# Optimization experiments

Measured on AMD Instinct MI355X. Metric: run time of the kernel, lower is better.

Reference implementation:

```python
import jax, jax.numpy as jnp
import numpy as np

B, N, IN_DIM, HID, EMB, E = 64, 2048, 128, 256, 64, 4194304
TOTAL = B * N


def _init(key, shape, fan_in):
    return jax.random.normal(key, shape, jnp.float32) / np.sqrt(fan_in).astype(np.float32)


def setup_inputs() -> dict:
    key = jax.random.key(0)
    ks = jax.random.split(key, 9)
    x = jax.random.normal(ks[0], (TOTAL, IN_DIM), jnp.float32)
    src = jax.random.randint(ks[1], (E,), 0, TOTAL)
    dst = jax.random.randint(ks[2], (E,), 0, TOTAL)
    return {
        "x": x,
        "src": src,
        "dst": dst,
        "num_nodes": TOTAL,
        "nodes_per_graph": N,
        "w_lin": _init(ks[3], (IN_DIM, HID), IN_DIM),
        "b_lin": jnp.zeros((HID,), jnp.float32),
        "w_c0": _init(ks[4], (HID, HID), HID),
        "b_c0": jnp.zeros((HID,), jnp.float32),
        "w_c1": _init(ks[5], (HID, HID), HID),
        "b_c1": jnp.zeros((HID,), jnp.float32),
        "w_emb": _init(ks[6], (HID, EMB), HID),
        "b_emb": jnp.zeros((EMB,), jnp.float32),
    }


def reference(x, src, dst, num_nodes, nodes_per_graph,
              w_lin, b_lin, w_c0, b_c0, w_c1, b_c1, w_emb, b_emb):
    # DGL GraphConv norm='both': deg clamped to min 1, symmetric normalization
    ones = jnp.ones(src.shape, x.dtype)
    out_deg = jax.ops.segment_sum(ones, src, num_segments=num_nodes)
    in_deg = jax.ops.segment_sum(ones, dst, num_segments=num_nodes)
    out_norm = jnp.maximum(out_deg, 1.0) ** -0.5  # [num_nodes]
    in_norm = jnp.maximum(in_deg, 1.0) ** -0.5

    def graph_conv(h, W, b):
        hs = h * out_norm[:, None]                                   # pre-norm by out-degree
        agg = jax.ops.segment_sum(hs[src], dst, num_segments=num_nodes)  # SpMM: sum messages
        return (agg * in_norm[:, None]) @ W + b                      # post-norm, then weight

    h = jax.nn.relu(x @ w_lin + b_lin)          # [total, HID]
    h = jax.nn.relu(graph_conv(h, w_c0, b_c0))  # residual=False for agg_style='node'
    h = jax.nn.relu(graph_conv(h, w_c1, b_c1))
    # agent node 0 of each graph in the batch: indices 0, N, 2N, ...
    agent = h[jnp.arange(0, num_nodes, nodes_per_graph)]  # [B, HID]
    return agent @ w_emb + b_emb                          # [B, EMB]
```

## Files before the change

kernel.cpp:

```cpp
#include <hip/hip_runtime.h>
#include <hip/hip_bf16.h>

#define TOTAL_N   131072
#define NEDGE     4194304
#define NPG       2048
#define IN_DIM_K  128
#define HID_K     256
#define EMB_K     64
#define NAGENT    64

#define F1CAP     4096
#define APACK     128
#define BCAP      96

#define G1        256
#define EPB1      (NEDGE / G1)
#define HWORDS    (TOTAL_N / 8)

#define SELB      256
#define EPB       (NEDGE / SELB)


#define ZERO_SPAN 34048

typedef float f32x4 __attribute__((ext_vector_type(4)));
typedef short bf16x8 __attribute__((ext_vector_type(8)));

__device__ inline unsigned short f2bf(float f) {
    unsigned int u = __float_as_uint(f);
    return (unsigned short)((u + 0x7FFFu + ((u >> 16) & 1u)) >> 16);
}

__global__ __launch_bounds__(1024) void k_outdeg_e0(
    const int* __restrict__ src, const int* __restrict__ dst,
    unsigned int* __restrict__ partial,
    unsigned int* __restrict__ bitmap,
    int* __restrict__ e0pack, int* __restrict__ e0cnt)
{
    __shared__ unsigned int hist[HWORDS];
    int t = threadIdx.x;
    #pragma unroll
    for (int i = 0; i < HWORDS / 1024; i++) hist[t + i * 1024] = 0u;
    __syncthreads();

    int ebase = blockIdx.x * EPB1;
    const int4* s4 = (const int4*)(src + ebase);
    const int4* d4 = (const int4*)(dst + ebase);
    #pragma unroll
    for (int i = 0; i < EPB1 / 4096; i++) {
        int4 sv = s4[i * 1024 + t];
        int4 dv = d4[i * 1024 + t];
        int ss[4] = {sv.x, sv.y, sv.z, sv.w};
        int dd[4] = {dv.x, dv.y, dv.z, dv.w};
        #pragma unroll
        for (int j = 0; j < 4; j++) {
            int s = ss[j], d = dd[j];
            atomicAdd(&hist[s >> 3], 1u << ((s & 7) * 4));
            if ((d & (NPG - 1)) == 0) {
                atomicOr(&bitmap[s >> 5], 1u << (s & 31));
                int a = d >> 11;
                int slot = atomicAdd(&e0cnt[a], 1);
                if (slot < APACK) e0pack[a * APACK + slot] = s;
            }
        }
    }
    __syncthreads();
    unsigned int* pout = partial + blockIdx.x * HWORDS;
    #pragma unroll
    for (int i = 0; i < HWORDS / 1024; i++) pout[t + i * 1024] = hist[t + i * 1024];
}

__global__ __launch_bounds__(1024) void k_auxred(
    const unsigned int* __restrict__ bitmap, int* __restrict__ loc,
    int* __restrict__ counters,
    const unsigned int* __restrict__ partial, unsigned int* __restrict__ out_deg,
    const float* __restrict__ wlin, unsigned short* __restrict__ wswz)
{
    int b = blockIdx.x;
    int t = threadIdx.x;
    if (b < 128) {
        __shared__ int cnt, gbase;
        if (t == 0) cnt = 0;
        __syncthreads();
        int v = b * 1024 + t;
        int f = (bitmap[v >> 5] >> (v & 31)) & 1u;
        int p = -1;
        if (f) p = atomicAdd(&cnt, 1);
        __syncthreads();
        if (t == 0) gbase = cnt ? atomicAdd(&counters[1], cnt) : 0;
        __syncthreads();
        int l = -1;
        if (p >= 0) { int id = gbase + p; if (id < F1CAP) l = id; }
        loc[v] = l;
    } else if (b < 256) {
        __shared__ unsigned int redE[8][128], redO[8][128];
        int wl = t & 127, gs = t >> 7;
        int w = (b - 128) * 128 + wl;
        unsigned int accE = 0, accO = 0;
        #pragma unroll 8
        for (int i = 0; i < 32; i++) {
            unsigned int v = partial[(gs * 32 + i) * HWORDS + w];
            accE += v & 0x0F0F0F0Fu;
            accO += (v >> 4) & 0x0F0F0F0Fu;
        }
        redE[gs][wl] = accE;
        redO[gs][wl] = accO;
        __syncthreads();
        if (gs == 0) {
            unsigned int sE = 0, sO = 0;
            #pragma unroll
            for (int j = 0; j < 8; j++) { sE += redE[j][wl]; sO += redO[j][wl]; }
            uint4 lo = make_uint4(sE & 255u, sO & 255u, (sE >> 8) & 255u, (sO >> 8) & 255u);
            uint4 hi = make_uint4((sE >> 16) & 255u, (sO >> 16) & 255u, (sE >> 24) & 255u, (sO >> 24) & 255u);
            ((uint4*)(out_deg + 8 * w))[0] = lo;
            ((uint4*)(out_deg + 8 * w))[1] = hi;
        }
    } else {
        int g = (b - 256) * 1024 + t;
        int lane = g & 63, ct = (g >> 6) & 15, kt = g >> 10;
        int colbase = ct * 16 + (lane & 15);
        int kbase = kt * 32 + (lane >> 4) * 8;
        unsigned short o[8];
        #pragma unroll
        for (int i = 0; i < 8; i++) o[i] = f2bf(wlin[(kbase + i) * HID_K + colbase]);
        *(ushort4*)(wswz + g * 8)     = make_ushort4(o[0], o[1], o[2], o[3]);
        *(ushort4*)(wswz + g * 8 + 4) = make_ushort4(o[4], o[5], o[6], o[7]);
    }
}

__global__ __launch_bounds__(1024) void k_e1_select(
    const int* __restrict__ src, const int* __restrict__ dst,
    const int* __restrict__ loc, const unsigned int* __restrict__ bitmap,
    int* __restrict__ inF1, int* __restrict__ es_bucket)
{
    __shared__ unsigned int bm[TOTAL_N / 32];
    int t = threadIdx.x;
    ((uint4*)bm)[t] = ((const uint4*)bitmap)[t];
    __syncthreads();

    int ebase = blockIdx.x * EPB;
    const int4* d4p = (const int4*)(dst + ebase);
    #pragma unroll
    for (int i = 0; i < EPB / 4096; i++) {
        int4 d4 = d4p[i * 1024 + t];
        int eidx = ebase + (i * 1024 + t) * 4;
        int dd[4] = {d4.x, d4.y, d4.z, d4.w};
        #pragma unroll
        for (int j = 0; j < 4; j++) {
            int d = dd[j];
            if ((bm[d >> 5] >> (d & 31)) & 1u) {
                int l = loc[d];
                if (l >= 0) {
                    int slot = atomicAdd(&inF1[l], 1);
                    if (slot < BCAP) es_bucket[l * BCAP + slot] = src[eidx + j];
                }
            }
        }
    }
}

__global__ __launch_bounds__(256) void k_h0agg(
    const float* __restrict__ x, const unsigned short* __restrict__ wswz,
    const float* __restrict__ blin, const int* __restrict__ es_bucket,
    const unsigned int* __restrict__ out_deg, const int* __restrict__ inF1,
    const int* __restrict__ counters, float* __restrict__ agg1)
{
    __shared__ unsigned short A[3 * 32][136];
    __shared__ float escs[3 * 32];
    __shared__ int rsrc[3 * 32];

    int nF1 = min(counters[1], F1CAP);
    int l = blockIdx.x;
    if (l >= nF1) return;
    int cnt = min(inF1[l], BCAP);
    int ntile = (cnt + 31) >> 5;
    int t = threadIdx.x;
    int lane = t & 63, wq = t >> 6;
    int cbase = lane & 15, rgrp = (lane >> 4) * 4;

    if (t < 96) {
        int s = (t < cnt) ? es_bucket[l * BCAP + t] : -1;
        rsrc[t] = s;
        escs[t] = (s >= 0) ? rsqrtf((float)max((int)out_deg[s], 1)) : 0.f;
    }
    __syncthreads();

    int nslots = (ntile * 32) * 32;
    for (int idx = t; idx < nslots; idx += 256) {
        int r = idx >> 5, q = idx & 31;
        int s = rsrc[r];
        float4 v = make_float4(0.f, 0.f, 0.f, 0.f);
        if (s >= 0) v = ((const float4*)(x + (long long)s * IN_DIM_K))[q];
        ushort4 h;
        h.x = f2bf(v.x); h.y = f2bf(v.y); h.z = f2bf(v.z); h.w = f2bf(v.w);
        *(ushort4*)&A[r][q * 4] = h;
    }
    __syncthreads();

    float bj[4];
    #pragma unroll
    for (int n = 0; n < 4; n++) bj[n] = blin[wq * 64 + n * 16 + cbase];

    float colacc[4] = {0.f, 0.f, 0.f, 0.f};

    for (int ti = 0; ti < ntile; ti++) {
        f32x4 acc[2][4];
        #pragma unroll
        for (int m = 0; m < 2; m++)
            #pragma unroll
            for (int n = 0; n < 4; n++) acc[m][n] = (f32x4){0.f, 0.f, 0.f, 0.f};

        const unsigned short* Ab = &A[ti * 32][0];
        #pragma unroll
        for (int kt = 0; kt < 4; kt++) {
            bf16x8 a0 = *(const bf16x8*)(Ab + ((lane & 15) * 136 + kt * 32 + (lane >> 4) * 8));
            bf16x8 a1 = *(const bf16x8*)(Ab + (((lane & 15) + 16) * 136 + kt * 32 + (lane >> 4) * 8));
            #pragma unroll
            for (int n = 0; n < 4; n++) {
                bf16x8 bf = *(const bf16x8*)(wswz + ((kt * 16 + wq * 4 + n) * 64 + lane) * 8);
                acc[0][n] = __builtin_amdgcn_mfma_f32_16x16x32_bf16(a0, bf, acc[0][n], 0, 0, 0);
                acc[1][n] = __builtin_amdgcn_mfma_f32_16x16x32_bf16(a1, bf, acc[1][n], 0, 0, 0);
            }
        }

        #pragma unroll
        for (int n = 0; n < 4; n++) {
            float part = 0.f;
            #pragma unroll
            for (int m = 0; m < 2; m++)
                #pragma unroll
                for (int j = 0; j < 4; j++) {
                    int row = m * 16 + rgrp + j;
                    part += fmaxf(acc[m][n][j] + bj[n], 0.f) * escs[ti * 32 + row];
                }
            part += __shfl_xor(part, 16);
            part += __shfl_xor(part, 32);
            colacc[n] += part;
        }
    }

    if (lane < 16) {
        #pragma unroll
        for (int n = 0; n < 4; n++)
            agg1[(long long)l * HID_K + wq * 64 + n * 16 + lane] = colacc[n];
    }
}

__global__ __launch_bounds__(256) void k_h1(
    const float* __restrict__ agg1, const float* __restrict__ wc0,
    const float* __restrict__ bc0,
    const int* __restrict__ inF1,
    const int* __restrict__ counters, float* __restrict__ h1)
{
    __shared__ float as[16][HID_K];
    __shared__ float ns[16];

    int nF1 = min(counters[1], F1CAP);
    int base = blockIdx.x * 16;
    if (base >= nF1) return;
    int t = threadIdx.x;

    if (t < 16) {
        int l = base + t;
        ns[t] = (l < nF1) ? rsqrtf((float)max(inF1[l], 1)) : 0.f;
    }
    __syncthreads();

    #pragma unroll
    for (int i = 0; i < 4; i++) {
        int idx = t + i * 256;
        int e = idx >> 6;
        int q = idx & 63;
        int l = base + e;
        float4 v = make_float4(0.f, 0.f, 0.f, 0.f);
        if (l < nF1) v = ((const float4*)(agg1 + (long long)l * HID_K))[q];
        float sc = ns[e];
        v.x *= sc; v.y *= sc; v.z *= sc; v.w *= sc;
        ((float4*)as[e])[q] = v;
    }
    __syncthreads();

    float acc[16];
    #pragma unroll
    for (int e = 0; e < 16; e++) acc[e] = 0.f;

    int j = t;
    for (int k = 0; k < HID_K; k += 4) {
        float w0 = wc0[(k + 0) * HID_K + j];
        float w1 = wc0[(k + 1) * HID_K + j];
        float w2 = wc0[(k + 2) * HID_K + j];
        float w3 = wc0[(k + 3) * HID_K + j];
        #pragma unroll
        for (int e = 0; e < 16; e++) {
            float4 av = *(const float4*)&as[e][k];
            acc[e] = fmaf(av.x, w0, acc[e]);
            acc[e] = fmaf(av.y, w1, acc[e]);
            acc[e] = fmaf(av.z, w2, acc[e]);
            acc[e] = fmaf(av.w, w3, acc[e]);
        }
    }

    float bj = bc0[j];
    #pragma unroll
    for (int e = 0; e < 16; e++) {
        int l = base + e;
        if (l < nF1) h1[(long long)l * HID_K + j] = fmaxf(acc[e] + bj, 0.f);
    }
}

__global__ __launch_bounds__(256) void k_final(
    const int* __restrict__ e0pack, const int* __restrict__ e0cnt,
    const int* __restrict__ loc, const unsigned int* __restrict__ out_deg,
    const float* __restrict__ h1,
    const float* __restrict__ wc1, const float* __restrict__ bc1,
    const float* __restrict__ wemb, const float* __restrict__ bemb,
    float* __restrict__ out)
{
    __shared__ float a_s[HID_K];
    __shared__ float h2[HID_K];
    __shared__ int   ls[APACK];
    __shared__ float scs[APACK];
    int a = blockIdx.x;
    int t = threadIdx.x;

    int n0 = e0cnt[a];
    int ne = min(n0, APACK);
    if (t < ne) {
        int s = e0pack[a * APACK + t];
        int l = loc[s];
        ls[t] = l;
        scs[t] = (l >= 0) ? rsqrtf((float)max((int)out_deg[s], 1)) : 0.f;
    }
    __syncthreads();

    float acc = 0.f;
    for (int i = 0; i < ne; i++) {
        int l = ls[i];
        if (l >= 0) acc = fmaf(scs[i], h1[(long long)l * HID_K + t], acc);
    }
    a_s[t] = acc * rsqrtf((float)max(n0, 1));
    __syncthreads();

    float h = 0.f;
    for (int k = 0; k < HID_K; k++)
        h = fmaf(a_s[k], wc1[k * HID_K + t], h);
    h2[t] = fmaxf(h + bc1[t], 0.f);
    __syncthreads();

    if (t < EMB_K) {
        float o = bemb[t];
        for (int k = 0; k < HID_K; k++)
            o = fmaf(h2[k], wemb[k * EMB_K + t], o);
        out[a * EMB_K + t] = o;
    }
}

extern "C" void kernel_launch(void* const* d_in, const int* in_sizes, int n_in,
                              void* d_out, int out_size, void* d_ws, size_t ws_size,
                              hipStream_t stream)
{
    const float* x    = (const float*)d_in[0];
    const int*   src  = (const int*)d_in[1];
    const int*   dst  = (const int*)d_in[2];
    const float* wlin = (const float*)d_in[5];
    const float* blin = (const float*)d_in[6];
    const float* wc0  = (const float*)d_in[7];
    const float* bc0  = (const float*)d_in[8];
    const float* wc1  = (const float*)d_in[9];
    const float* bc1  = (const float*)d_in[10];
    const float* wemb = (const float*)d_in[11];
    const float* bemb = (const float*)d_in[12];
    float* out = (float*)d_out;

    char* ws = (char*)d_ws;
    int*            counters  = (int*)(ws + 0);
    int*            inF1      = (int*)(ws + 1024);
    int*            e0cnt     = (int*)(ws + 17408);
    unsigned int*   bitmap    = (unsigned int*)(ws + 17664);
    int*            loc       = (int*)(ws + 65536);
    int*            e0pack    = (int*)(ws + 589824);
    int*            es_bucket = (int*)(ws + 622592);
    unsigned int*   out_deg   = (unsigned int*)(ws + 2195456);
    unsigned short* wswz      = (unsigned short*)(ws + 2719744);
    float*          h1        = (float*)(ws + 2785280);
    float*          agg1      = (float*)(ws + 6979584);
    unsigned int*   partial   = (unsigned int*)(ws + 11173888);

    hipMemsetAsync(ws, 0, ZERO_SPAN, stream);

    k_outdeg_e0<<<G1, 1024, 0, stream>>>(src, dst, partial, bitmap, e0pack, e0cnt);
    k_auxred<<<260, 1024, 0, stream>>>(bitmap, loc, counters,
                                       partial, out_deg, wlin, wswz);
    k_e1_select<<<SELB, 1024, 0, stream>>>(src, dst, loc, bitmap,
                                           inF1, es_bucket);
    k_h0agg<<<F1CAP, 256, 0, stream>>>(x, wswz, blin, es_bucket, out_deg,
                                       inF1, counters, agg1);
    k_h1<<<F1CAP / 16, 256, 0, stream>>>(agg1, wc0, bc0, inF1, counters, h1);
    k_final<<<NAGENT, 256, 0, stream>>>(e0pack, e0cnt, loc, out_deg, h1,
                                        wc1, bc1, wemb, bemb, out);
}
```

Baseline: 117.0 us.

## Deduplicate layer-0 source nodes before computing h0, then gather-aggregate

Instead of computing the first linear layer once per incoming edge of each frontier node, the selection pass now marks unique source nodes in a second bitmap. A new compaction kernel assigns them dense ids. h0 is then computed once per unique source into a global buffer, and a separate kernel sums the pre-normalised rows per frontier node. This removes repeated MFMA work and x reads for sources shared by several edges. In exchange it adds atomicOr traffic, two extra launches, and a large intermediate h0 buffer that must be written and then gathered back.

```diff
diff --git a/kernel.cpp b/kernel.cpp
--- a/kernel.cpp
+++ b/kernel.cpp
@@ -10,6 +10,7 @@
 #define NAGENT    64
 
 #define F1CAP     4096
+#define F2CAP     81920
 #define APACK     128
 #define BCAP      96
 
@@ -21,7 +22,7 @@
 #define EPB       (NEDGE / SELB)
 
 
-#define ZERO_SPAN 34048
+#define ZERO_SPAN 50304
 
 typedef float f32x4 __attribute__((ext_vector_type(4)));
 typedef short bf16x8 __attribute__((ext_vector_type(8)));
@@ -131,7 +132,8 @@
 __global__ __launch_bounds__(1024) void k_e1_select(
     const int* __restrict__ src, const int* __restrict__ dst,
     const int* __restrict__ loc, const unsigned int* __restrict__ bitmap,
-    int* __restrict__ inF1, int* __restrict__ es_bucket)
+    int* __restrict__ inF1, int* __restrict__ es_bucket,
+    unsigned int* __restrict__ bitmap2)
 {
     __shared__ unsigned int bm[TOTAL_N / 32];
     int t = threadIdx.x;
@@ -151,99 +153,138 @@
             if ((bm[d >> 5] >> (d & 31)) & 1u) {
                 int l = loc[d];
                 if (l >= 0) {
+                    int s = src[eidx + j];
+                    atomicOr(&bitmap2[s >> 5], 1u << (s & 31));
                     int slot = atomicAdd(&inF1[l], 1);
-                    if (slot < BCAP) es_bucket[l * BCAP + slot] = src[eidx + j];
+                    if (slot < BCAP) es_bucket[l * BCAP + slot] = s;
                 }
             }
         }
     }
 }
 
-__global__ __launch_bounds__(256) void k_h0agg(
+__global__ __launch_bounds__(1024) void k_compact2(
+    const unsigned int* __restrict__ bitmap2, int* __restrict__ loc2,
+    int* __restrict__ nodeOf2, int* __restrict__ counters)
+{
+    __shared__ int cnt, gbase;
+    int t = threadIdx.x;
+    if (t == 0) cnt = 0;
+    __syncthreads();
+    int v = blockIdx.x * 1024 + t;
+    int f = (bitmap2[v >> 5] >> (v & 31)) & 1u;
+    int p = -1;
+    if (f) p = atomicAdd(&cnt, 1);
+    __syncthreads();
+    if (t == 0) gbase = cnt ? atomicAdd(&counters[2], cnt) : 0;
+    __syncthreads();
+    int l = -1;
+    if (p >= 0) {
+        int id = gbase + p;
+        if (id < F2CAP) { l = id; nodeOf2[id] = v; }
+    }
+    loc2[v] = l;
+}
+
+__global__ __launch_bounds__(256) void k_h0f2(
     const float* __restrict__ x, const unsigned short* __restrict__ wswz,
-    const float* __restrict__ blin, const int* __restrict__ es_bucket,
-    const unsigned int* __restrict__ out_deg, const int* __restrict__ inF1,
+    const float* __restrict__ blin, const int* __restrict__ nodeOf2,
+    const unsigned int* __restrict__ out_deg, const int* __restrict__ counters,
+    float* __restrict__ h0f2)
+{
+    __shared__ unsigned short A[32][136];
+    __shared__ float escs[32];
+    __shared__ int rsrc[32];
+
+    int nF2 = min(counters[2], F2CAP);
+    int base = blockIdx.x * 32;
+    if (base >= nF2) return;
+    int t = threadIdx.x;
+    int lane = t & 63, wq = t >> 6;
+    int cbase = lane & 15, rgrp = (lane >> 4) * 4;
+
+    if (t < 32) {
+        int r = base + t;
+        int s = (r < nF2) ? nodeOf2[r] : -1;
+        rsrc[t] = s;
+        escs[t] = (s >= 0) ? rsqrtf((float)max((int)out_deg[s], 1)) : 0.f;
+    }
+    __syncthreads();
+
+    #pragma unroll
+    for (int i = 0; i < 4; i++) {
+        int idx = t + i * 256;
+        int rr = idx >> 5, q = idx & 31;
+        int s = rsrc[rr];
+        float4 v = make_float4(0.f, 0.f, 0.f, 0.f);
+        if (s >= 0) v = ((const float4*)(x + (long long)s * IN_DIM_K))[q];
+        ushort4 h;
+        h.x = f2bf(v.x); h.y = f2bf(v.y); h.z = f2bf(v.z); h.w = f2bf(v.w);
+        *(ushort4*)&A[rr][q * 4] = h;
+    }
+    __syncthreads();
+
+    f32x4 acc[2][4];
+    #pragma unroll
+    for (int m = 0; m < 2; m++)
+        #pragma unroll
+        for (int n = 0; n < 4; n++) acc[m][n] = (f32x4){0.f, 0.f, 0.f, 0.f};
+
+    const unsigned short* Ab = &A[0][0];
+    #pragma unroll
+    for (int kt = 0; kt < 4; kt++) {
+        bf16x8 a0 = *(const bf16x8*)(Ab + ((lane & 15) * 136 + kt * 32 + (lane >> 4) * 8));
+        bf16x8 a1 = *(const bf16x8*)(Ab + (((lane & 15) + 16) * 136 + kt * 32 + (lane >> 4) * 8));
+        #pragma unroll
+        for (int n = 0; n < 4; n++) {
+            bf16x8 bf = *(const bf16x8*)(wswz + ((kt * 16 + wq * 4 + n) * 64 + lane) * 8);
+            acc[0][n] = __builtin_amdgcn_mfma_f32_16x16x32_bf16(a0, bf, acc[0][n], 0, 0, 0);
+            acc[1][n] = __builtin_amdgcn_mfma_f32_16x16x32_bf16(a1, bf, acc[1][n], 0, 0, 0);
+        }
+    }
+
+    #pragma unroll
+    for (int n = 0; n < 4; n++) {
+        float bj = blin[wq * 64 + n * 16 + cbase];
+        #pragma unroll
+        for (int m = 0; m < 2; m++)
+            #pragma unroll
+            for (int j = 0; j < 4; j++) {
+                int row = m * 16 + rgrp + j;
+                int r = base + row;
+                if (r < nF2) {
+                    int col = wq * 64 + n * 16 + cbase;
+                    h0f2[(long long)r * HID_K + col] =
+                        fmaxf(acc[m][n][j] + bj, 0.f) * escs[row];
+                }
+            }
+    }
+}
+
+__global__ __launch_bounds__(256) void k_agg(
+    const int* __restrict__ es_bucket, const int* __restrict__ inF1,
+    const int* __restrict__ loc2, const float* __restrict__ h0f2,
     const int* __restrict__ counters, float* __restrict__ agg1)
 {
-    __shared__ unsigned short A[3 * 32][136];
-    __shared__ float escs[3 * 32];
-    __shared__ int rsrc[3 * 32];
-
+    __shared__ int lr[BCAP];
     int nF1 = min(counters[1], F1CAP);
     int l = blockIdx.x;
     if (l >= nF1) return;
     int cnt = min(inF1[l], BCAP);
-    int ntile = (cnt + 31) >> 5;
-    int t = threadIdx.x;
-    int lane = t & 63, wq = t >> 6;
-    int cbase = lane & 15, rgrp = (lane >> 4) * 4;
-
-    if (t < 96) {
+    int t = threadIdx.x;
+
+    if (t < BCAP) {
         int s = (t < cnt) ? es_bucket[l * BCAP + t] : -1;
-        rsrc[t] = s;
-        escs[t] = (s >= 0) ? rsqrtf((float)max((int)out_deg[s], 1)) : 0.f;
-    }
-    __syncthreads();
-
-    int nslots = (ntile * 32) * 32;
-    for (int idx = t; idx < nslots; idx += 256) {
-        int r = idx >> 5, q = idx & 31;
-        int s = rsrc[r];
-        float4 v = make_float4(0.f, 0.f, 0.f, 0.f);
-        if (s >= 0) v = ((const float4*)(x + (long long)s * IN_DIM_K))[q];
-        ushort4 h;
-        h.x = f2bf(v.x); h.y = f2bf(v.y); h.z = f2bf(v.z); h.w = f2bf(v.w);
-        *(ushort4*)&A[r][q * 4] = h;
-    }
-    __syncthreads();
-
-    float bj[4];
-    #pragma unroll
-    for (int n = 0; n < 4; n++) bj[n] = blin[wq * 64 + n * 16 + cbase];
-
-    float colacc[4] = {0.f, 0.f, 0.f, 0.f};
-
-    for (int ti = 0; ti < ntile; ti++) {
-        f32x4 acc[2][4];
-        #pragma unroll
-        for (int m = 0; m < 2; m++)
-            #pragma unroll
-            for (int n = 0; n < 4; n++) acc[m][n] = (f32x4){0.f, 0.f, 0.f, 0.f};
-
-        const unsigned short* Ab = &A[ti * 32][0];
-        #pragma unroll
-        for (int kt = 0; kt < 4; kt++) {
-            bf16x8 a0 = *(const bf16x8*)(Ab + ((lane & 15) * 136 + kt * 32 + (lane >> 4) * 8));
-            bf16x8 a1 = *(const bf16x8*)(Ab + (((lane & 15) + 16) * 136 + kt * 32 + (lane >> 4) * 8));
-            #pragma unroll
-            for (int n = 0; n < 4; n++) {
-                bf16x8 bf = *(const bf16x8*)(wswz + ((kt * 16 + wq * 4 + n) * 64 + lane) * 8);
-                acc[0][n] = __builtin_amdgcn_mfma_f32_16x16x32_bf16(a0, bf, acc[0][n], 0, 0, 0);
-                acc[1][n] = __builtin_amdgcn_mfma_f32_16x16x32_bf16(a1, bf, acc[1][n], 0, 0, 0);
-            }
-        }
-
-        #pragma unroll
-        for (int n = 0; n < 4; n++) {
-            float part = 0.f;
-            #pragma unroll
-            for (int m = 0; m < 2; m++)
-                #pragma unroll
-                for (int j = 0; j < 4; j++) {
-                    int row = m * 16 + rgrp + j;
-                    part += fmaxf(acc[m][n][j] + bj[n], 0.f) * escs[ti * 32 + row];
-                }
-            part += __shfl_xor(part, 16);
-            part += __shfl_xor(part, 32);
-            colacc[n] += part;
-        }
-    }
-
-    if (lane < 16) {
-        #pragma unroll
-        for (int n = 0; n < 4; n++)
-            agg1[(long long)l * HID_K + wq * 64 + n * 16 + lane] = colacc[n];
-    }
+        lr[t] = (s >= 0) ? loc2[s] : -1;
+    }
+    __syncthreads();
+
+    float sum = 0.f;
+    for (int i = 0; i < cnt; i++) {
+        int r = lr[i];
+        if (r >= 0) sum += h0f2[(long long)r * HID_K + t];
+    }
+    agg1[(long long)l * HID_K + t] = sum;
 }
 
 __global__ __launch_bounds__(256) void k_h1(
@@ -377,6 +418,7 @@
     int*            inF1      = (int*)(ws + 1024);
     int*            e0cnt     = (int*)(ws + 17408);
     unsigned int*   bitmap    = (unsigned int*)(ws + 17664);
+    unsigned int*   bitmap2   = (unsigned int*)(ws + 33920);
     int*            loc       = (int*)(ws + 65536);
     int*            e0pack    = (int*)(ws + 589824);
     int*            es_bucket = (int*)(ws + 622592);
@@ -384,7 +426,10 @@
     unsigned short* wswz      = (unsigned short*)(ws + 2719744);
     float*          h1        = (float*)(ws + 2785280);
     float*          agg1      = (float*)(ws + 6979584);
-    unsigned int*   partial   = (unsigned int*)(ws + 11173888);
+    int*            loc2      = (int*)(ws + 11173888);
+    int*            nodeOf2   = (int*)(ws + 11698176);
+    float*          h0f2      = (float*)(ws + 12025856);
+    unsigned int*   partial   = (unsigned int*)(ws + 95911936);
 
     hipMemsetAsync(ws, 0, ZERO_SPAN, stream);
 
@@ -392,9 +437,13 @@
     k_auxred<<<260, 1024, 0, stream>>>(bitmap, loc, counters,
                                        partial, out_deg, wlin, wswz);
     k_e1_select<<<SELB, 1024, 0, stream>>>(src, dst, loc, bitmap,
-                                           inF1, es_bucket);
-    k_h0agg<<<F1CAP, 256, 0, stream>>>(x, wswz, blin, es_bucket, out_deg,
-                                       inF1, counters, agg1);
+                                           inF1, es_bucket, bitmap2);
+    k_compact2<<<TOTAL_N / 1024, 1024, 0, stream>>>(bitmap2, loc2, nodeOf2,
+                                                    counters);
+    k_h0f2<<<F2CAP / 32, 256, 0, stream>>>(x, wswz, blin, nodeOf2, out_deg,
+                                           counters, h0f2);
+    k_agg<<<F1CAP, 256, 0, stream>>>(es_bucket, inF1, loc2, h0f2,
+                                     counters, agg1);
     k_h1<<<F1CAP / 16, 256, 0, stream>>>(agg1, wc0, bc0, inF1, counters, h1);
     k_final<<<NAGENT, 256, 0, stream>>>(e0pack, e0cnt, loc, out_deg, h1,
                                         wc1, bc1, wemb, bemb, out);
```

New measurement: 149.1 us. 27.4% more time.

## Compute out-degrees only for nodes reachable from agents via global atomics

Applied to the files above, without the earlier changes.

Drops the full shared-memory nibble histogram of out-degrees and its per-block partial buffer and reduction. Instead it marks second-hop source nodes in a second bitmap during edge selection. A new pass then counts out-degree only for sources flagged in either bitmap, using global atomics. This removes the large partial write and read and the LDS histogram, at the cost of another full pass over src and a larger memset.

```diff
diff --git a/kernel.cpp b/kernel.cpp
--- a/kernel.cpp
+++ b/kernel.cpp
@@ -15,13 +15,9 @@
 
 #define G1        256
 #define EPB1      (NEDGE / G1)
-#define HWORDS    (TOTAL_N / 8)
-
-#define SELB      256
-#define EPB       (NEDGE / SELB)
-
-
-#define ZERO_SPAN 34048
+
+
+#define ZERO_SPAN 574592
 
 typedef float f32x4 __attribute__((ext_vector_type(4)));
 typedef short bf16x8 __attribute__((ext_vector_type(8)));
@@ -31,32 +27,24 @@
     return (unsigned short)((u + 0x7FFFu + ((u >> 16) & 1u)) >> 16);
 }
 
-__global__ __launch_bounds__(1024) void k_outdeg_e0(
+__global__ __launch_bounds__(1024) void k_dst_scan(
     const int* __restrict__ src, const int* __restrict__ dst,
-    unsigned int* __restrict__ partial,
     unsigned int* __restrict__ bitmap,
     int* __restrict__ e0pack, int* __restrict__ e0cnt)
 {
-    __shared__ unsigned int hist[HWORDS];
-    int t = threadIdx.x;
-    #pragma unroll
-    for (int i = 0; i < HWORDS / 1024; i++) hist[t + i * 1024] = 0u;
-    __syncthreads();
-
+    int t = threadIdx.x;
     int ebase = blockIdx.x * EPB1;
-    const int4* s4 = (const int4*)(src + ebase);
     const int4* d4 = (const int4*)(dst + ebase);
     #pragma unroll
     for (int i = 0; i < EPB1 / 4096; i++) {
-        int4 sv = s4[i * 1024 + t];
         int4 dv = d4[i * 1024 + t];
-        int ss[4] = {sv.x, sv.y, sv.z, sv.w};
+        int eidx = ebase + (i * 1024 + t) * 4;
         int dd[4] = {dv.x, dv.y, dv.z, dv.w};
         #pragma unroll
         for (int j = 0; j < 4; j++) {
-            int s = ss[j], d = dd[j];
-            atomicAdd(&hist[s >> 3], 1u << ((s & 7) * 4));
+            int d = dd[j];
             if ((d & (NPG - 1)) == 0) {
+                int s = src[eidx + j];
                 atomicOr(&bitmap[s >> 5], 1u << (s & 31));
                 int a = d >> 11;
                 int slot = atomicAdd(&e0cnt[a], 1);
@@ -64,16 +52,11 @@
             }
         }
     }
-    __syncthreads();
-    unsigned int* pout = partial + blockIdx.x * HWORDS;
-    #pragma unroll
-    for (int i = 0; i < HWORDS / 1024; i++) pout[t + i * 1024] = hist[t + i * 1024];
-}
-
-__global__ __launch_bounds__(1024) void k_auxred(
+}
+
+__global__ __launch_bounds__(1024) void k_aux(
     const unsigned int* __restrict__ bitmap, int* __restrict__ loc,
     int* __restrict__ counters,
-    const unsigned int* __restrict__ partial, unsigned int* __restrict__ out_deg,
     const float* __restrict__ wlin, unsigned short* __restrict__ wswz)
 {
     int b = blockIdx.x;
@@ -92,31 +75,8 @@
         int l = -1;
         if (p >= 0) { int id = gbase + p; if (id < F1CAP) l = id; }
         loc[v] = l;
-    } else if (b < 256) {
-        __shared__ unsigned int redE[8][128], redO[8][128];
-        int wl = t & 127, gs = t >> 7;
-        int w = (b - 128) * 128 + wl;
-        unsigned int accE = 0, accO = 0;
-        #pragma unroll 8
-        for (int i = 0; i < 32; i++) {
-            unsigned int v = partial[(gs * 32 + i) * HWORDS + w];
-            accE += v & 0x0F0F0F0Fu;
-            accO += (v >> 4) & 0x0F0F0F0Fu;
-        }
-        redE[gs][wl] = accE;
-        redO[gs][wl] = accO;
-        __syncthreads();
-        if (gs == 0) {
-            unsigned int sE = 0, sO = 0;
-            #pragma unroll
-            for (int j = 0; j < 8; j++) { sE += redE[j][wl]; sO += redO[j][wl]; }
-            uint4 lo = make_uint4(sE & 255u, sO & 255u, (sE >> 8) & 255u, (sO >> 8) & 255u);
-            uint4 hi = make_uint4((sE >> 16) & 255u, (sO >> 16) & 255u, (sE >> 24) & 255u, (sO >> 24) & 255u);
-            ((uint4*)(out_deg + 8 * w))[0] = lo;
-            ((uint4*)(out_deg + 8 * w))[1] = hi;
-        }
     } else {
-        int g = (b - 256) * 1024 + t;
+        int g = (b - 128) * 1024 + t;
         int lane = g & 63, ct = (g >> 6) & 15, kt = g >> 10;
         int colbase = ct * 16 + (lane & 15);
         int kbase = kt * 32 + (lane >> 4) * 8;
@@ -131,17 +91,18 @@
 __global__ __launch_bounds__(1024) void k_e1_select(
     const int* __restrict__ src, const int* __restrict__ dst,
     const int* __restrict__ loc, const unsigned int* __restrict__ bitmap,
-    int* __restrict__ inF1, int* __restrict__ es_bucket)
+    int* __restrict__ inF1, int* __restrict__ es_bucket,
+    unsigned int* __restrict__ bitmap2)
 {
     __shared__ unsigned int bm[TOTAL_N / 32];
     int t = threadIdx.x;
     ((uint4*)bm)[t] = ((const uint4*)bitmap)[t];
     __syncthreads();
 
-    int ebase = blockIdx.x * EPB;
+    int ebase = blockIdx.x * EPB1;
     const int4* d4p = (const int4*)(dst + ebase);
     #pragma unroll
-    for (int i = 0; i < EPB / 4096; i++) {
+    for (int i = 0; i < EPB1 / 4096; i++) {
         int4 d4 = d4p[i * 1024 + t];
         int eidx = ebase + (i * 1024 + t) * 4;
         int dd[4] = {d4.x, d4.y, d4.z, d4.w};
@@ -151,10 +112,39 @@
             if ((bm[d >> 5] >> (d & 31)) & 1u) {
                 int l = loc[d];
                 if (l >= 0) {
+                    int s = src[eidx + j];
+                    atomicOr(&bitmap2[s >> 5], 1u << (s & 31));
                     int slot = atomicAdd(&inF1[l], 1);
-                    if (slot < BCAP) es_bucket[l * BCAP + slot] = src[eidx + j];
+                    if (slot < BCAP) es_bucket[l * BCAP + slot] = s;
                 }
             }
+        }
+    }
+}
+
+__global__ __launch_bounds__(1024) void k_deg(
+    const int* __restrict__ src,
+    const unsigned int* __restrict__ bitmap, const unsigned int* __restrict__ bitmap2,
+    unsigned int* __restrict__ out_deg)
+{
+    __shared__ unsigned int bm[TOTAL_N / 32];
+    __shared__ unsigned int bm2[TOTAL_N / 32];
+    int t = threadIdx.x;
+    ((uint4*)bm)[t]  = ((const uint4*)bitmap)[t];
+    ((uint4*)bm2)[t] = ((const uint4*)bitmap2)[t];
+    __syncthreads();
+
+    int ebase = blockIdx.x * EPB1;
+    const int4* s4 = (const int4*)(src + ebase);
+    #pragma unroll
+    for (int i = 0; i < EPB1 / 4096; i++) {
+        int4 sv = s4[i * 1024 + t];
+        int ss[4] = {sv.x, sv.y, sv.z, sv.w};
+        #pragma unroll
+        for (int j = 0; j < 4; j++) {
+            int s = ss[j];
+            if (((bm[s >> 5] | bm2[s >> 5]) >> (s & 31)) & 1u)
+                atomicAdd(&out_deg[s], 1u);
         }
     }
 }
@@ -377,22 +367,22 @@
     int*            inF1      = (int*)(ws + 1024);
     int*            e0cnt     = (int*)(ws + 17408);
     unsigned int*   bitmap    = (unsigned int*)(ws + 17664);
-    int*            loc       = (int*)(ws + 65536);
-    int*            e0pack    = (int*)(ws + 589824);
-    int*            es_bucket = (int*)(ws + 622592);
-    unsigned int*   out_deg   = (unsigned int*)(ws + 2195456);
+    unsigned int*   bitmap2   = (unsigned int*)(ws + 34048);
+    unsigned int*   out_deg   = (unsigned int*)(ws + 50304);
+    int*            loc       = (int*)(ws + 589824);
+    int*            e0pack    = (int*)(ws + 1114112);
+    int*            es_bucket = (int*)(ws + 1146880);
     unsigned short* wswz      = (unsigned short*)(ws + 2719744);
     float*          h1        = (float*)(ws + 2785280);
     float*          agg1      = (float*)(ws + 6979584);
-    unsigned int*   partial   = (unsigned int*)(ws + 11173888);
 
     hipMemsetAsync(ws, 0, ZERO_SPAN, stream);
 
-    k_outdeg_e0<<<G1, 1024, 0, stream>>>(src, dst, partial, bitmap, e0pack, e0cnt);
-    k_auxred<<<260, 1024, 0, stream>>>(bitmap, loc, counters,
-                                       partial, out_deg, wlin, wswz);
-    k_e1_select<<<SELB, 1024, 0, stream>>>(src, dst, loc, bitmap,
-                                           inF1, es_bucket);
+    k_dst_scan<<<G1, 1024, 0, stream>>>(src, dst, bitmap, e0pack, e0cnt);
+    k_aux<<<132, 1024, 0, stream>>>(bitmap, loc, counters, wlin, wswz);
+    k_e1_select<<<G1, 1024, 0, stream>>>(src, dst, loc, bitmap,
+                                         inF1, es_bucket, bitmap2);
+    k_deg<<<G1, 1024, 0, stream>>>(src, bitmap, bitmap2, out_deg);
     k_h0agg<<<F1CAP, 256, 0, stream>>>(x, wswz, blin, es_bucket, out_deg,
                                        inF1, counters, agg1);
     k_h1<<<F1CAP / 16, 256, 0, stream>>>(agg1, wc0, bc0, inF1, counters, h1);
```

Measured after the change: 193.4 us. 1.65x slower.
